# Kernel tuning notes

Measured on AMD Instinct MI355X. Metric: run time of the kernel, lower is better.

## Reference

```python
import jax, jax.numpy as jnp
import numpy as np

B, H, E, DFF, K = 4096, 1024, 8, 4096, 2
THRESH = 0.1


def setup_inputs() -> dict:
    key = jax.random.key(0)
    ks = jax.random.split(key, 8)
    g = lambda k, shape, scale: (jax.random.normal(k, shape, jnp.float32) * scale)
    return {
        "x": jax.random.normal(ks[0], (B, H), jnp.float32),
        "gate_w1": g(ks[1], (H, H // 2), 0.03),
        "gate_b1": jnp.zeros((H // 2,), jnp.float32),
        "gate_w2": g(ks[2], (H // 2, E), 0.06),
        "gate_b2": jnp.zeros((E,), jnp.float32),
        "exp_w1": g(ks[3], (E, H, DFF), 0.03),
        "exp_b1": jnp.zeros((E, DFF), jnp.float32),
        "exp_w2": g(ks[4], (E, DFF, H), 0.015),
        "exp_b2": jnp.zeros((E, H), jnp.float32),
        "proj_w": g(ks[5], (E, H, H), 0.03),
        "blend": jnp.asarray(0.0, jnp.float32),
    }


def reference(x, gate_w1, gate_b1, gate_w2, gate_b2,
              exp_w1, exp_b1, exp_w2, exp_b2, proj_w, blend):
    # PathGate: Linear -> SiLU -> Linear, logits (B, E)
    logits = jax.nn.silu(x @ gate_w1 + gate_b1) @ gate_w2 + gate_b2
    # eval mode (training=False): plain softmax (Markov bayes adjustment = 0)
    gate_weights = jax.nn.softmax(logits, axis=-1)

    # top-k selection with firing threshold
    top_vals, top_idx = jax.lax.top_k(gate_weights, K)        # (B, K)
    keep = top_vals > THRESH                                  # (B, K)
    # scatter kept top-k weights back to dense (B, E) dispatch weights
    onehot = jax.nn.one_hot(top_idx, E, dtype=gate_weights.dtype)  # (B, K, E)
    w_full = jnp.sum(jnp.where(keep[..., None], top_vals[..., None], 0.0) * onehot, axis=1)  # (B, E)

    # per-expert MLP + out_proj, weighted combine (loop over fixed E experts)
    combined = jnp.zeros_like(x)
    for e in range(E):
        h = jax.nn.silu(x @ exp_w1[e] + exp_b1[e]) @ exp_w2[e] + exp_b2[e]  # (B, H)
        combined = combined + w_full[:, e:e + 1] * (h @ proj_w[e])

    total_weight = jnp.sum(w_full, axis=-1)                   # (B,)
    fired = total_weight > 0
    safe_tw = jnp.where(fired, total_weight, 1.0)
    combined = jnp.where(fired[:, None], combined / safe_tw[:, None], x)

    alpha = jax.nn.sigmoid(blend)
    output = alpha * combined + (1.0 - alpha) * x
    return output, gate_weights
```

## Files before the change

kernel.cpp:

```cpp
#include <hip/hip_runtime.h>
#include <hip/hip_bf16.h>
#include <cmath>

constexpr int NB = 4096;
constexpr int NH = 1024;
constexpr int NE = 8;
constexpr int NF = 4096;
constexpr int NG = 512;
constexpr float THRESH = 0.1f;
constexpr int PAD_ROWS = 128;
constexpr size_t MAXS = (size_t)2 * NB;
constexpr size_t ROWS = MAXS + PAD_ROWS;


typedef float  f32x4  __attribute__((ext_vector_type(4)));
typedef __bf16 bf16x8 __attribute__((ext_vector_type(8)));
typedef __bf16 bf16x4 __attribute__((ext_vector_type(4)));

typedef __attribute__((address_space(1))) void gvoid_t;
typedef __attribute__((address_space(3))) void svoid_t;

__device__ __forceinline__ void gl_lds16(const void* g, void* l)
{
    __builtin_amdgcn_global_load_lds((gvoid_t*)g, (svoid_t*)l, 16, 0, 0);
}

__device__ __forceinline__ float silu_f(float v) { return v / (1.f + expf(-v)); }

__global__ void k_sentinel(float* out, float code)
{
    if (threadIdx.x == 0 && blockIdx.x == 0) out[0] = code;
}

__device__ __forceinline__ void tconv_body(
    const float* __restrict__ I, __bf16* __restrict__ O, int R, int C,
    int bx, int by, float* smem)
{
    const int r0 = by * 64, c0 = bx * 64;
    const int tid = threadIdx.x;
    const int rr = tid >> 4;
    const int c4 = tid & 15;
#pragma unroll
    for (int i = 0; i < 4; i++) {
        int r = i * 16 + rr;
        f32x4 v = *(const f32x4*)&I[(size_t)(r0 + r) * C + c0 + c4 * 4];
#pragma unroll
        for (int j = 0; j < 4; j++) smem[r * 65 + c4 * 4 + j] = v[j];
    }
    __syncthreads();
    const int cw = tid >> 3;
    const int rp = tid & 7;
#pragma unroll
    for (int i = 0; i < 2; i++) {
        int c = cw + i * 32;
        bf16x8 v;
#pragma unroll
        for (int j = 0; j < 8; j++)
            v[j] = (__bf16)smem[(rp * 8 + j) * 65 + c];
        *(bf16x8*)&O[(size_t)(c0 + c) * R + r0 + rp * 8] = v;
    }
}

__global__ __launch_bounds__(256) void k_prework(
    const float* __restrict__ x, const float* __restrict__ gw1,
    const float* __restrict__ gb1, float* __restrict__ hidden,
    const float* __restrict__ ew1, __bf16* __restrict__ Wt1,
    const float* __restrict__ ew2, __bf16* __restrict__ Wt2,
    const float* __restrict__ pw,  __bf16* __restrict__ Wtp)
{
    __shared__ float smem[64 * 65];
    int id = blockIdx.x;

    if (id < 512) {
        float* As = smem;
        float* Bs = smem + 16 * 68;
        const int tid = threadIdx.x;
        const int r0 = (id >> 3) * 64, c0 = (id & 7) * 64;
        const int tx = tid & 15, ty = tid >> 4;
        float acc[4][4] = {};
        for (int k0 = 0; k0 < NH; k0 += 16) {
#pragma unroll
            for (int i = 0; i < 4; i++) {
                int e = tid + i * 256;
                int m = e >> 4, kk = e & 15;
                As[kk * 68 + m] = x[(size_t)(r0 + m) * NH + k0 + kk];
            }
#pragma unroll
            for (int i = 0; i < 4; i++) {
                int e = tid + i * 256;
                int kk = e >> 6, n = e & 63;
                Bs[kk * 64 + n] = gw1[(size_t)(k0 + kk) * NG + c0 + n];
            }
            __syncthreads();
#pragma unroll
            for (int kk = 0; kk < 16; kk++) {
                f32x4 a = *(const f32x4*)&As[kk * 68 + ty * 4];
                f32x4 b = *(const f32x4*)&Bs[kk * 64 + tx * 4];
#pragma unroll
                for (int i = 0; i < 4; i++)
#pragma unroll
                    for (int j = 0; j < 4; j++)
                        acc[i][j] = fmaf(a[i], b[j], acc[i][j]);
            }
            __syncthreads();
        }
#pragma unroll
        for (int i = 0; i < 4; i++) {
            int row = r0 + ty * 4 + i;
            f32x4 o;
#pragma unroll
            for (int j = 0; j < 4; j++)
                o[j] = silu_f(acc[i][j] + gb1[c0 + tx * 4 + j]);
            *(f32x4*)&hidden[(size_t)row * NG + c0 + tx * 4] = o;
        }
        return;
    }
    id -= 512;
    if (id < 8192) {
        int bx = id & 63, by = (id >> 6) & 15, e = id >> 10;
        tconv_body(ew1 + (size_t)e * NH * NF, Wt1 + (size_t)e * NH * NF,
                   NH, NF, bx, by, smem);
        return;
    }
    id -= 8192;
    if (id < 8192) {
        int bx = id & 15, by = (id >> 4) & 63, e = id >> 10;
        tconv_body(ew2 + (size_t)e * NF * NH, Wt2 + (size_t)e * NF * NH,
                   NF, NH, bx, by, smem);
        return;
    }
    id -= 8192;
    {
        int bx = id & 15, by = (id >> 4) & 15, e = id >> 8;
        tconv_body(pw + (size_t)e * NH * NH, Wtp + (size_t)e * NH * NH,
                   NH, NH, bx, by, smem);
    }
}

__global__ __launch_bounds__(64) void k_router(
    const float* __restrict__ hidden, const float* __restrict__ w2,
    const float* __restrict__ b2, float* __restrict__ gw_out,
    int* __restrict__ count, int* __restrict__ slot_row,
    float* __restrict__ slot_w, float* __restrict__ row_total,
    int* __restrict__ row_fired)
{
    const int r = blockIdx.x;
    const int l = threadIdx.x;
    float pe[NE] = {};
    for (int k = l; k < NG; k += 64) {
        float h = hidden[(size_t)r * NG + k];
        const float* wr = w2 + (size_t)k * NE;
#pragma unroll
        for (int e = 0; e < NE; e++) pe[e] += h * wr[e];
    }
#pragma unroll
    for (int e = 0; e < NE; e++) {
#pragma unroll
        for (int m = 1; m < 64; m <<= 1) pe[e] += __shfl_xor(pe[e], m);
    }
    float logit[NE];
    float mx = -1e30f;
#pragma unroll
    for (int e = 0; e < NE; e++) { logit[e] = pe[e] + b2[e]; mx = fmaxf(mx, logit[e]); }
    float w[NE], s = 0.f;
#pragma unroll
    for (int e = 0; e < NE; e++) { w[e] = expf(logit[e] - mx); s += w[e]; }
    float inv = 1.f / s;
#pragma unroll
    for (int e = 0; e < NE; e++) w[e] *= inv;
    if (l < NE) gw_out[(size_t)r * NE + l] = w[l];

    int i1 = 0; float v1 = w[0];
#pragma unroll
    for (int e = 1; e < NE; e++) if (w[e] > v1) { v1 = w[e]; i1 = e; }
    int i2 = -1; float v2 = -1.f;
#pragma unroll
    for (int e = 0; e < NE; e++) if (e != i1 && w[e] > v2) { v2 = w[e]; i2 = e; }

    bool k1 = v1 > THRESH, k2 = v2 > THRESH;
    float total = (k1 ? v1 : 0.f) + (k2 ? v2 : 0.f);
    if (l == 0) {
        row_total[r] = total;
        row_fired[r] = (total > 0.f) ? 1 : 0;
        if (k1) { int p = atomicAdd(&count[i1], 1); slot_row[i1 * NB + p] = r; slot_w[i1 * NB + p] = v1; }
        if (k2) { int p = atomicAdd(&count[i2], 1); slot_row[i2 * NB + p] = r; slot_w[i2 * NB + p] = v2; }
    }
}

__global__ void k_offsets(const int* __restrict__ count, int* __restrict__ offs)
{
    if (threadIdx.x == 0 && blockIdx.x == 0) {
        int s = 0;
        for (int e = 0; e < NE; e++) { offs[e] = s; s += count[e]; }
    }
}

__global__ __launch_bounds__(256) void k_xc(
    const float* __restrict__ x, const int* __restrict__ count,
    const int* __restrict__ offs, const int* __restrict__ slot_row,
    __bf16* __restrict__ Xc)
{
    const int s = blockIdx.x;
    int e = 0;
#pragma unroll
    for (int i = 1; i < NE; i++) if (s >= offs[i]) e = i;
    if (s >= offs[NE - 1] + count[NE - 1]) return;
    const int r = slot_row[e * NB + (s - offs[e])];
    const float* src = x + (size_t)r * NH;
    __bf16* dst = Xc + (size_t)s * NH;
    const int t = threadIdx.x;
    f32x4 v = *(const f32x4*)(src + t * 4);
    bf16x4 o;
#pragma unroll
    for (int j = 0; j < 4; j++) o[j] = (__bf16)v[j];
    *(bf16x4*)(dst + t * 4) = o;
}

template<int ACT, int OM>
__global__ __launch_bounds__(256) void k_gemm2(
    const __bf16* __restrict__ A, int lda,
    const __bf16* __restrict__ Wt, size_t wstride,
    const float* __restrict__ bias, int bstride,
    __bf16* __restrict__ outB, float* __restrict__ outF,
    int N, int Kd, int X,
    const int* __restrict__ count, const int* __restrict__ offs,
    const int* __restrict__ slot_row, const float* __restrict__ slot_w)
{
    const int bx = blockIdx.x;
    const int e  = bx / X;
    const int n0 = (bx % X) * 128;
    const int cnt = count[e];
    const int row0 = blockIdx.y * 128;
    if (row0 >= cnt) return;
    const int off = offs[e];
    const __bf16* W = Wt + (size_t)e * wstride;
    const int tid = threadIdx.x;
    const int lane = tid & 63, wid = tid >> 6;
    const int wm = (wid >> 1) * 64, wn = (wid & 1) * 64;
    const int arow0 = off + row0;

    __shared__ __align__(16) unsigned char sA[16384];
    __shared__ __align__(16) unsigned char sB[16384];

    f32x4 acc[4][4];
#pragma unroll
    for (int mi = 0; mi < 4; mi++)
#pragma unroll
        for (int ni = 0; ni < 4; ni++)
            acc[mi][ni] = (f32x4){0.f, 0.f, 0.f, 0.f};

    const int sub = lane >> 3;
    const int kcx = (lane & 7) ^ sub;

    for (int k0 = 0; k0 < Kd; k0 += 64) {
#pragma unroll
        for (int i = 0; i < 4; i++) {
            int c = wid * 4 + i;
            int row = c * 8 + sub;
            gl_lds16(A + (size_t)(arow0 + row) * lda + k0 + kcx * 8,
                     sA + c * 1024 + lane * 16);
        }
#pragma unroll
        for (int i = 0; i < 4; i++) {
            int c = wid * 4 + i;
            int n = c * 8 + sub;
            gl_lds16(W + (size_t)(n0 + n) * Kd + k0 + kcx * 8,
                     sB + c * 1024 + lane * 16);
        }
        __syncthreads();
#pragma unroll
        for (int ks = 0; ks < 2; ks++) {
            bf16x8 af[4], bfr[4];
            const int kb = ks * 64 + ((lane >> 4) << 4);
#pragma unroll
            for (int mi = 0; mi < 4; mi++) {
                int row = wm + mi * 16 + (lane & 15);
                af[mi] = *(const bf16x8*)(sA + row * 128 + (kb ^ ((row & 7) << 4)));
            }
#pragma unroll
            for (int ni = 0; ni < 4; ni++) {
                int row = wn + ni * 16 + (lane & 15);
                bfr[ni] = *(const bf16x8*)(sB + row * 128 + (kb ^ ((row & 7) << 4)));
            }
#pragma unroll
            for (int mi = 0; mi < 4; mi++)
#pragma unroll
                for (int ni = 0; ni < 4; ni++)
                    acc[mi][ni] = __builtin_amdgcn_mfma_f32_16x16x32_bf16(
                        af[mi], bfr[ni], acc[mi][ni], 0, 0, 0);
        }
        __syncthreads();
    }

    const int q = lane >> 4, cl = lane & 15;
#pragma unroll
    for (int mi = 0; mi < 4; mi++) {
#pragma unroll
        for (int r = 0; r < 4; r++) {
            int srow = row0 + wm + mi * 16 + q * 4 + r;
            if (srow >= cnt) continue;
            if (OM == 0) {
#pragma unroll
                for (int ni = 0; ni < 4; ni++) {
                    int col = n0 + wn + ni * 16 + cl;
                    float vv = acc[mi][ni][r] + bias[(size_t)e * bstride + col];
                    if (ACT) vv = silu_f(vv);
                    outB[(size_t)(off + srow) * N + col] = (__bf16)vv;
                }
            } else {
                int grow = slot_row[e * NB + srow];
                float wsl = slot_w[e * NB + srow];
#pragma unroll
                for (int ni = 0; ni < 4; ni++) {
                    int col = n0 + wn + ni * 16 + cl;
                    atomicAdd(&outF[(size_t)grow * NH + col], wsl * acc[mi][ni][r]);
                }
            }
        }
    }
}

__global__ __launch_bounds__(256) void k_final(
    const float* __restrict__ x,
    const float* __restrict__ row_total, const int* __restrict__ row_fired,
    const float* __restrict__ blend, float* __restrict__ out)
{
    int idx = blockIdx.x * 256 + threadIdx.x;
    int r = idx >> 8;
    int c = (idx & 255) << 2;
    float alpha = 1.f / (1.f + expf(-blend[0]));
    f32x4 cb = *(const f32x4*)(out + (size_t)r * NH + c);
    f32x4 xv = *(const f32x4*)(x + (size_t)r * NH + c);
    int fired = row_fired[r];
    float inv_t = fired ? (1.f / row_total[r]) : 0.f;
    f32x4 o;
#pragma unroll
    for (int j = 0; j < 4; j++)
        o[j] = fired ? (alpha * (cb[j] * inv_t) + (1.f - alpha) * xv[j]) : xv[j];
    *(f32x4*)&out[(size_t)r * NH + c] = o;
}

extern "C" void kernel_launch(void* const* d_in, const int* in_sizes, int n_in,
                              void* d_out, int out_size, void* d_ws, size_t ws_size,
                              hipStream_t stream)
{
    float* out_main = (float*)d_out;
    float* gw_out   = (float*)d_out + (size_t)NB * NH;

    static const long long EXP[11] = {
        (long long)NB * NH, (long long)NH * NG, NG, (long long)NG * NE, NE,
        (long long)NE * NH * NF, (long long)NE * NF,
        (long long)NE * NF * NH, (long long)NE * NH,
        (long long)NE * NH * NH, 1
    };
    bool ok = (n_in == 11);
    if (ok)
        for (int i = 0; i < 11; i++)
            if ((long long)in_sizes[i] != EXP[i]) { ok = false; break; }
    if (!ok) {
        k_sentinel<<<1, 1, 0, stream>>>((float*)d_out, 2000.f + n_in);
        return;
    }

    const float* x    = (const float*)d_in[0];
    const float* gw1  = (const float*)d_in[1];
    const float* gb1  = (const float*)d_in[2];
    const float* gw2  = (const float*)d_in[3];
    const float* gb2  = (const float*)d_in[4];
    const float* ew1  = (const float*)d_in[5];
    const float* eb1  = (const float*)d_in[6];
    const float* ew2  = (const float*)d_in[7];
    const float* eb2  = (const float*)d_in[8];
    const float* pw   = (const float*)d_in[9];
    const float* blnd = (const float*)d_in[10];

    size_t need = 0;
    size_t off_meta   = need;   need += 512;
    size_t off_srow   = need;   need += (size_t)NE * NB * 4;
    size_t off_sw     = need;   need += (size_t)NE * NB * 4;
    size_t off_total  = need;   need += (size_t)NB * 4;
    size_t off_fired  = need;   need += (size_t)NB * 4;
    size_t off_hidden = need;   need += (size_t)NB * NG * 4;
    size_t a_xc  = need;
    size_t a_h1  = a_xc + ROWS * NH * 2;
    size_t a_h2  = a_h1 + ROWS * NF * 2;
    size_t a_w1  = a_h2 + ROWS * NH * 2;
    size_t a_w2  = a_w1 + (size_t)NE * NH * NF * 2;
    size_t a_wp  = a_w2 + (size_t)NE * NF * NH * 2;
    size_t need_A = a_wp + (size_t)NE * NH * NH * 2;

    char* ws = (char*)d_ws;
    int*   count     = (int*)(ws + off_meta);
    int*   offs      = count + 8;
    int*   slot_row  = (int*)(ws + off_srow);
    float* slot_w    = (float*)(ws + off_sw);
    float* row_total = (float*)(ws + off_total);
    int*   row_fired = (int*)(ws + off_fired);
    float* hidden    = (float*)(ws + off_hidden);

    if (ws_size < need_A) {
        k_sentinel<<<1, 1, 0, stream>>>((float*)d_out,
                                        1000.f + (float)(ws_size >> 20));
        return;
    }
    __bf16* Xc  = (__bf16*)(ws + a_xc);
    __bf16* H1  = (__bf16*)(ws + a_h1);
    __bf16* H2  = (__bf16*)(ws + a_h2);
    __bf16* Wt1 = (__bf16*)(ws + a_w1);
    __bf16* Wt2 = (__bf16*)(ws + a_w2);
    __bf16* Wtp = (__bf16*)(ws + a_wp);

    hipMemsetAsync(count, 0, 512, stream);
    hipMemsetAsync(out_main, 0, (size_t)NB * NH * 4, stream);

    k_prework<<<dim3(512 + 8192 + 8192 + 2048), 256, 0, stream>>>(
        x, gw1, gb1, hidden, ew1, Wt1, ew2, Wt2, pw, Wtp);

    k_router<<<dim3(NB), 64, 0, stream>>>(hidden, gw2, gb2, gw_out,
                                          count, slot_row, slot_w, row_total, row_fired);
    k_offsets<<<1, 1, 0, stream>>>(count, offs);
    k_xc<<<dim3((int)MAXS), 256, 0, stream>>>(x, count, offs, slot_row, Xc);

    k_gemm2<1, 0><<<dim3(32 * NE, NB / 128), 256, 0, stream>>>(
        Xc, NH, Wt1, (size_t)NH * NF, eb1, NF,
        H1, nullptr, NF, NH, 32, count, offs, slot_row, slot_w);
    k_gemm2<0, 0><<<dim3(8 * NE, NB / 128), 256, 0, stream>>>(
        H1, NF, Wt2, (size_t)NF * NH, eb2, NH,
        H2, nullptr, NH, NF, 8, count, offs, slot_row, slot_w);
    k_gemm2<0, 1><<<dim3(8 * NE, NB / 128), 256, 0, stream>>>(
        H2, NH, Wtp, (size_t)NH * NH, eb2 , 0,
        nullptr, out_main, NH, NH, 8, count, offs, slot_row, slot_w);

    k_final<<<dim3(NB * NH / 1024), 256, 0, stream>>>(x, row_total,
                                                      row_fired, blnd, out_main);
}
```

Before: 546.3 us.

## Overlap weight transposes with expert GEMMs and drop offsets kernel

Moves the bf16 transpose-conversion of the second-layer and projection weights out of the prework kernel. Each is now done by extra blocks appended to the grid of the preceding expert GEMM, so that conversion overlaps with GEMM compute. The one-thread offsets kernel is removed, and expert offsets are recomputed from counts inside k_xc and the GEMMs. This trades a kernel launch and a serialized conversion phase for shared LDS use and extra blocks competing with the GEMM blocks.

```diff
diff --git a/kernel.cpp b/kernel.cpp
--- a/kernel.cpp
+++ b/kernel.cpp
@@ -61,12 +61,10 @@
     }
 }
 
-__global__ __launch_bounds__(256) void k_prework(
+__global__ __launch_bounds__(256) void k_gate_ew1(
     const float* __restrict__ x, const float* __restrict__ gw1,
     const float* __restrict__ gb1, float* __restrict__ hidden,
-    const float* __restrict__ ew1, __bf16* __restrict__ Wt1,
-    const float* __restrict__ ew2, __bf16* __restrict__ Wt2,
-    const float* __restrict__ pw,  __bf16* __restrict__ Wtp)
+    const float* __restrict__ ew1, __bf16* __restrict__ Wt1)
 {
     __shared__ float smem[64 * 65];
     int id = blockIdx.x;
@@ -116,25 +114,9 @@
         return;
     }
     id -= 512;
-    if (id < 8192) {
-        int bx = id & 63, by = (id >> 6) & 15, e = id >> 10;
-        tconv_body(ew1 + (size_t)e * NH * NF, Wt1 + (size_t)e * NH * NF,
-                   NH, NF, bx, by, smem);
-        return;
-    }
-    id -= 8192;
-    if (id < 8192) {
-        int bx = id & 15, by = (id >> 4) & 63, e = id >> 10;
-        tconv_body(ew2 + (size_t)e * NF * NH, Wt2 + (size_t)e * NF * NH,
-                   NF, NH, bx, by, smem);
-        return;
-    }
-    id -= 8192;
-    {
-        int bx = id & 15, by = (id >> 4) & 15, e = id >> 8;
-        tconv_body(pw + (size_t)e * NH * NH, Wtp + (size_t)e * NH * NH,
-                   NH, NH, bx, by, smem);
-    }
+    int bx = id & 63, by = (id >> 6) & 15, e = id >> 10;
+    tconv_body(ew1 + (size_t)e * NH * NF, Wt1 + (size_t)e * NH * NF,
+               NH, NF, bx, by, smem);
 }
 
 __global__ __launch_bounds__(64) void k_router(
@@ -187,25 +169,19 @@
     }
 }
 
-__global__ void k_offsets(const int* __restrict__ count, int* __restrict__ offs)
-{
-    if (threadIdx.x == 0 && blockIdx.x == 0) {
-        int s = 0;
-        for (int e = 0; e < NE; e++) { offs[e] = s; s += count[e]; }
-    }
-}
-
 __global__ __launch_bounds__(256) void k_xc(
     const float* __restrict__ x, const int* __restrict__ count,
-    const int* __restrict__ offs, const int* __restrict__ slot_row,
-    __bf16* __restrict__ Xc)
+    const int* __restrict__ slot_row, __bf16* __restrict__ Xc)
 {
     const int s = blockIdx.x;
-    int e = 0;
-#pragma unroll
-    for (int i = 1; i < NE; i++) if (s >= offs[i]) e = i;
-    if (s >= offs[NE - 1] + count[NE - 1]) return;
-    const int r = slot_row[e * NB + (s - offs[e])];
+    int acc = 0, e = -1, off = 0;
+#pragma unroll
+    for (int i = 0; i < NE; i++) {
+        if (s >= acc) { e = i; off = acc; }
+        acc += count[i];
+    }
+    if (s >= acc) return;
+    const int r = slot_row[e * NB + (s - off)];
     const float* src = x + (size_t)r * NH;
     __bf16* dst = Xc + (size_t)s * NH;
     const int t = threadIdx.x;
@@ -223,24 +199,42 @@
     const float* __restrict__ bias, int bstride,
     __bf16* __restrict__ outB, float* __restrict__ outF,
     int N, int Kd, int X,
-    const int* __restrict__ count, const int* __restrict__ offs,
-    const int* __restrict__ slot_row, const float* __restrict__ slot_w)
-{
+    const int* __restrict__ count,
+    const int* __restrict__ slot_row, const float* __restrict__ slot_w,
+    const float* __restrict__ tcI, __bf16* __restrict__ tcO,
+    int tcR, int tcC)
+{
+    __shared__ __align__(16) unsigned char lds[32768];
     const int bx = blockIdx.x;
+
+    if (bx >= X * NE) {
+        if (tcI) {
+            int id = (bx - X * NE) * gridDim.y + blockIdx.y;
+            int xT = tcC >> 6, yT = tcR >> 6;
+            int per = xT * yT;
+            int e = id / per, rem = id - e * per;
+            int byy = rem / xT, bxx = rem - byy * xT;
+            tconv_body(tcI + (size_t)e * tcR * tcC, tcO + (size_t)e * tcR * tcC,
+                       tcR, tcC, bxx, byy, (float*)lds);
+        }
+        return;
+    }
+
+    unsigned char* sA = lds;
+    unsigned char* sB = lds + 16384;
+
     const int e  = bx / X;
     const int n0 = (bx % X) * 128;
     const int cnt = count[e];
     const int row0 = blockIdx.y * 128;
     if (row0 >= cnt) return;
-    const int off = offs[e];
+    int off = 0;
+    for (int i = 0; i < NE; i++) off += (i < e) ? count[i] : 0;
     const __bf16* W = Wt + (size_t)e * wstride;
     const int tid = threadIdx.x;
     const int lane = tid & 63, wid = tid >> 6;
     const int wm = (wid >> 1) * 64, wn = (wid & 1) * 64;
     const int arow0 = off + row0;
-
-    __shared__ __align__(16) unsigned char sA[16384];
-    __shared__ __align__(16) unsigned char sB[16384];
 
     f32x4 acc[4][4];
 #pragma unroll
@@ -391,7 +385,6 @@
 
     char* ws = (char*)d_ws;
     int*   count     = (int*)(ws + off_meta);
-    int*   offs      = count + 8;
     int*   slot_row  = (int*)(ws + off_srow);
     float* slot_w    = (float*)(ws + off_sw);
     float* row_total = (float*)(ws + off_total);
@@ -413,23 +406,25 @@
     hipMemsetAsync(count, 0, 512, stream);
     hipMemsetAsync(out_main, 0, (size_t)NB * NH * 4, stream);
 
-    k_prework<<<dim3(512 + 8192 + 8192 + 2048), 256, 0, stream>>>(
-        x, gw1, gb1, hidden, ew1, Wt1, ew2, Wt2, pw, Wtp);
+    k_gate_ew1<<<dim3(512 + 8192), 256, 0, stream>>>(
+        x, gw1, gb1, hidden, ew1, Wt1);
 
     k_router<<<dim3(NB), 64, 0, stream>>>(hidden, gw2, gb2, gw_out,
                                           count, slot_row, slot_w, row_total, row_fired);
-    k_offsets<<<1, 1, 0, stream>>>(count, offs);
-    k_xc<<<dim3((int)MAXS), 256, 0, stream>>>(x, count, offs, slot_row, Xc);
-
-    k_gemm2<1, 0><<<dim3(32 * NE, NB / 128), 256, 0, stream>>>(
+    k_xc<<<dim3((int)MAXS), 256, 0, stream>>>(x, count, slot_row, Xc);
+
+    k_gemm2<1, 0><<<dim3(256 + 256, NB / 128), 256, 0, stream>>>(
         Xc, NH, Wt1, (size_t)NH * NF, eb1, NF,
-        H1, nullptr, NF, NH, 32, count, offs, slot_row, slot_w);
-    k_gemm2<0, 0><<<dim3(8 * NE, NB / 128), 256, 0, stream>>>(
+        H1, nullptr, NF, NH, 32, count, slot_row, slot_w,
+        ew2, Wt2, NF, NH);
+    k_gemm2<0, 0><<<dim3(64 + 64, NB / 128), 256, 0, stream>>>(
         H1, NF, Wt2, (size_t)NF * NH, eb2, NH,
-        H2, nullptr, NH, NF, 8, count, offs, slot_row, slot_w);
-    k_gemm2<0, 1><<<dim3(8 * NE, NB / 128), 256, 0, stream>>>(
+        H2, nullptr, NH, NF, 8, count, slot_row, slot_w,
+        pw, Wtp, NH, NH);
+    k_gemm2<0, 1><<<dim3(64, NB / 128), 256, 0, stream>>>(
         H2, NH, Wtp, (size_t)NH * NH, eb2 , 0,
-        nullptr, out_main, NH, NH, 8, count, offs, slot_row, slot_w);
+        nullptr, out_main, NH, NH, 8, count, slot_row, slot_w,
+        nullptr, nullptr, 0, 64);
 
     k_final<<<dim3(NB * NH / 1024), 256, 0, stream>>>(x, row_total,
                                                       row_fired, blnd, out_main);
```

New measurement: 564.9 us. +3.4%, slower.
